# Performance work log

Hardware: AMD Instinct MI355X
Metric: run time of the kernel (lower is better)

Reference implementation:

```python
import jax, jax.numpy as jnp
import numpy as np

HEADS = 16
HEAD_DIM = 128


def rotate_half(x):
    x1, x2 = jnp.split(x, 2, axis=-1)
    return jnp.concatenate((-x2, x1), axis=-1)


def setup_inputs() -> dict:
    key = jax.random.key(0)
    ks = jax.random.split(key, 8)
    b, s, h = 2, 2048, 2048
    x = jax.random.normal(ks[0], (b, s, h), dtype=jnp.float32)
    attention_mask = jnp.zeros((1, 1, s, s), dtype=jnp.float32)
    alibi = jax.random.normal(ks[1], (1, HEADS, 1, s), dtype=jnp.float32)
    freqs = jax.random.normal(ks[2], (1, 1, s, HEAD_DIM), dtype=jnp.float32)
    scale = 1.0 / np.sqrt(h)
    Wq = jax.random.normal(ks[3], (h, h), dtype=jnp.float32) * scale
    Wk = jax.random.normal(ks[4], (h, h), dtype=jnp.float32) * scale
    Wv = jax.random.normal(ks[5], (h, h), dtype=jnp.float32) * scale
    Wo = jax.random.normal(ks[6], (h, h), dtype=jnp.float32) * scale
    return {"x": x, "attention_mask": attention_mask, "alibi": alibi,
            "freqs": freqs, "Wq": Wq, "Wk": Wk, "Wv": Wv, "Wo": Wo}


def reference(x, attention_mask, alibi, freqs, Wq, Wk, Wv, Wo):
    b, s, hidden = x.shape
    # torch Linear: y = x @ W.T (weight shape [out, in])
    def proj(W):
        y = x @ W.T
        return y.reshape(b, s, HEADS, HEAD_DIM).transpose(0, 2, 1, 3)  # [b,H,s,d]
    q, k, v = proj(Wq), proj(Wk), proj(Wv)
    cos, sin = jnp.cos(freqs), jnp.sin(freqs)
    q = q * cos + rotate_half(q) * sin
    k = k * cos + rotate_half(k) * sin
    scores = jnp.einsum('bhqd,bhkd->bhqk', q, k) / np.sqrt(HEAD_DIM)
    scores = scores + attention_mask + alibi
    attn = jax.nn.softmax(scores, axis=-1)
    out = jnp.einsum('bhqk,bhkd->bhqd', attn, v)
    out = out.transpose(0, 2, 1, 3).reshape(b, s, hidden)
    return out @ Wo.T
```

## Files before the change

kernel.cpp:

```cpp
#include <hip/hip_runtime.h>
#include <math.h>

typedef __attribute__((ext_vector_type(8))) short short8;
typedef __attribute__((ext_vector_type(4))) float f32x4;
typedef __attribute__((ext_vector_type(4))) unsigned short us4;
typedef __attribute__((ext_vector_type(4))) float fl4;

#define B_ 2
#define S_ 2048
#define H_ 16
#define D_ 128
#define HID 2048

__device__ __forceinline__ unsigned short f2bf(float f){
  unsigned u = __builtin_bit_cast(unsigned, f);
  u += 0x7fffu + ((u >> 16) & 1u);
  return (unsigned short)(u >> 16);
}
__device__ __forceinline__ float bf2f(unsigned short u){
  unsigned x = ((unsigned)u) << 16;
  return __builtin_bit_cast(float, x);
}
__device__ __forceinline__ int cvtpk(float lo, float hi){
  int r; asm("v_cvt_pk_bf16_f32 %0, %1, %2" : "=v"(r) : "v"(lo), "v"(hi)); return r;
}

__device__ __forceinline__ void g2lds16(const unsigned short* g, unsigned short* l){
  __builtin_amdgcn_global_load_lds(
      (const __attribute__((address_space(1))) unsigned int*)g,
      (__attribute__((address_space(3))) unsigned int*)l, 16, 0, 0);
}

__global__ void cvt_k(const float* __restrict__ src, unsigned short* __restrict__ dst){
  int i = (blockIdx.x * 256 + threadIdx.x) * 4;
  fl4 v = *(const fl4*)(src + i);
  us4 o;
  #pragma unroll
  for (int t = 0; t < 4; t++) o[t] = f2bf(v[t]);
  *(us4*)(dst + i) = o;
}

__global__ void tab_k(const float* __restrict__ freqs, float* __restrict__ ctab,
                      float* __restrict__ stab){
  int i = blockIdx.x * 256 + threadIdx.x;
  float f = freqs[i];
  ctab[i] = cosf(f);
  stab[i] = sinf(f);
}

template<int EPI>
__global__ __launch_bounds__(256) void gemm_k(
    const unsigned short* __restrict__ A,
    const unsigned short* __restrict__ B0,
    const unsigned short* __restrict__ B1,
    unsigned short* __restrict__ O0,
    unsigned short* __restrict__ O1,
    float* __restrict__ Of)
{
  __shared__ __align__(16) unsigned short As[2][128 * 32];
  __shared__ __align__(16) unsigned short Bs[2][128 * 32];
  const int tid = threadIdx.x;
  const int l = tid & 63, lg = l >> 4, lr = l & 15;
  const int w = tid >> 6, wm = w & 1, wn = w >> 1;
  const int m0 = blockIdx.x * 128, n0 = blockIdx.y * 128;
  const unsigned short* Bm = (EPI == 1 && blockIdx.z == 1) ? B1 : B0;

  f32x4 acc[4][4];
  #pragma unroll
  for (int i = 0; i < 4; i++)
    #pragma unroll
    for (int j = 0; j < 4; j++)
      acc[i][j] = f32x4{0.f, 0.f, 0.f, 0.f};

  const unsigned short* gA = A  + (size_t)(m0 + (tid >> 2)) * HID + (tid & 3) * 8;
  const unsigned short* gB = Bm + (size_t)(n0 + (tid >> 2)) * HID + (tid & 3) * 8;

  #define GSTAGE(buf, kt) do {                                   \
    g2lds16(gA + (kt),            As[buf] + tid * 8);            \
    g2lds16(gA + 64 * HID + (kt), As[buf] + 2048 + tid * 8);     \
    g2lds16(gB + (kt),            Bs[buf] + tid * 8);            \
    g2lds16(gB + 64 * HID + (kt), Bs[buf] + 2048 + tid * 8);     \
  } while (0)

  GSTAGE(0, 0);
  __syncthreads();
  int cur = 0;
  for (int t = 0; t < 64; t++){
    if (t < 63) GSTAGE(cur ^ 1, (t + 1) * 32);
    short8 aF[4], bF[4];
    #pragma unroll
    for (int mi = 0; mi < 4; mi++)
      aF[mi] = *(const short8*)(As[cur] + (wm * 64 + mi * 16 + lr) * 32 + lg * 8);
    #pragma unroll
    for (int ni = 0; ni < 4; ni++)
      bF[ni] = *(const short8*)(Bs[cur] + (wn * 64 + ni * 16 + lr) * 32 + lg * 8);
    #pragma unroll
    for (int mi = 0; mi < 4; mi++)
      #pragma unroll
      for (int ni = 0; ni < 4; ni++)
        acc[mi][ni] = __builtin_amdgcn_mfma_f32_16x16x32_bf16(aF[mi], bF[ni], acc[mi][ni], 0, 0, 0);
    __syncthreads();
    cur ^= 1;
  }
  #undef GSTAGE

  if (EPI == 1){
    unsigned short* O = blockIdx.z ? O1 : O0;
    #pragma unroll
    for (int mi = 0; mi < 4; mi++)
      #pragma unroll
      for (int r = 0; r < 4; r++){
        int i = m0 + wm * 64 + mi * 16 + lg * 4 + r;
        int b = i >> 11, s = i & 2047;
        #pragma unroll
        for (int ni = 0; ni < 4; ni++){
          int j = n0 + wn * 64 + ni * 16 + lr;
          int h = j >> 7, d = j & 127;
          O[((size_t)(b * H_ + h) * S_ + s) * D_ + d] = f2bf(acc[mi][ni][r]);
        }
      }
  } else if (EPI == 2){
    #pragma unroll
    for (int mi = 0; mi < 4; mi++)
      #pragma unroll
      for (int r = 0; r < 4; r++){
        int gi = m0 + wm * 64 + mi * 16 + lg * 4 + r;
        int h = gi >> 7, d = gi & 127;
        #pragma unroll
        for (int ni = 0; ni < 4; ni++){
          int gj = n0 + wn * 64 + ni * 16 + lr;
          int b = gj >> 11, s = gj & 2047;
          O0[((size_t)(b * H_ + h) * D_ + d) * S_ + s] = f2bf(acc[mi][ni][r]);
        }
      }
  } else {
    #pragma unroll
    for (int mi = 0; mi < 4; mi++)
      #pragma unroll
      for (int r = 0; r < 4; r++){
        int i = m0 + wm * 64 + mi * 16 + lg * 4 + r;
        #pragma unroll
        for (int ni = 0; ni < 4; ni++){
          int j = n0 + wn * 64 + ni * 16 + lr;
          Of[(size_t)i * HID + j] = acc[mi][ni][r];
        }
      }
  }
}

__global__ void rope_k(unsigned short* __restrict__ Q, unsigned short* __restrict__ K,
                       const float* __restrict__ ctab, const float* __restrict__ stab){
  int idx = blockIdx.x * 256 + threadIdx.x;
  unsigned short* P = (idx >= (1 << 20)) ? K : Q;
  int e  = idx & ((1 << 20) - 1);
  int g  = e & 15;
  int s  = (e >> 4) & 2047;
  int bh = e >> 15;
  int d0 = g * 4;
  size_t base = ((size_t)bh * S_ + s) * D_;
  us4 qa = *(us4*)(P + base + d0);
  us4 qb = *(us4*)(P + base + d0 + 64);
  fl4 ca = *(const fl4*)(ctab + s * D_ + d0);
  fl4 sa = *(const fl4*)(stab + s * D_ + d0);
  fl4 cb = *(const fl4*)(ctab + s * D_ + d0 + 64);
  fl4 sb = *(const fl4*)(stab + s * D_ + d0 + 64);
  us4 oa, ob;
  #pragma unroll
  for (int t = 0; t < 4; t++){
    float xa = bf2f(qa[t]), xb = bf2f(qb[t]);
    oa[t] = f2bf(xa * ca[t] - xb * sa[t]);
    ob[t] = f2bf(xb * cb[t] + xa * sb[t]);
  }
  *(us4*)(P + base + d0)      = oa;
  *(us4*)(P + base + d0 + 64) = ob;
}

__global__ __launch_bounds__(256) void attn_k(
    const unsigned short* __restrict__ Q,
    const unsigned short* __restrict__ Kg,
    const unsigned short* __restrict__ Vt,
    const float* __restrict__ mask,
    const float* __restrict__ alibi,
    unsigned short* __restrict__ Ctx)
{
  __shared__ __align__(16) unsigned short Kl[2][64 * 128];
  __shared__ __align__(16) unsigned short Vl[2][128 * 64];
  const int tid = threadIdx.x;
  const int l = tid & 63, lg = l >> 4, lr = l & 15;
  const int w = tid >> 6;
  const int bh = blockIdx.y, b = bh >> 4, h = bh & 15;
  const int q0 = blockIdx.x * 64 + w * 16;
  const size_t hb = (size_t)bh * S_ * D_;
  const float* mrow = mask + (size_t)(q0 + lr) * S_;
  const float* al = alibi + h * S_;
  const int sidx = (l & 48) + ((l & 48) >> 2);
  const float SCL2E = 0.08838834764831845f * 1.4426950408889634f;
  const float L2E = 1.4426950408889634f;

  const int kswz = (((tid & 15) ^ ((tid >> 4) & 7)) * 8);
  const unsigned short* gK = Kg + hb + (size_t)(tid >> 4) * D_ + kswz;
  const int vswz = (((tid & 7) ^ ((tid >> 3) & 7)) * 8);
  const unsigned short* gV = Vt + hb + (size_t)(tid >> 3) * S_ + vswz;

  #define ASTAGE(buf, kv)  do {                                            \
    g2lds16(gK + (size_t)((kv))      * D_, Kl[buf] + tid * 8);             \
    g2lds16(gK + (size_t)((kv) + 16) * D_, Kl[buf] + 2048 + tid * 8);      \
    g2lds16(gK + (size_t)((kv) + 32) * D_, Kl[buf] + 4096 + tid * 8);      \
    g2lds16(gK + (size_t)((kv) + 48) * D_, Kl[buf] + 6144 + tid * 8);      \
    g2lds16(gV + (kv),                     Vl[buf] + tid * 8);             \
    g2lds16(gV + 32 * S_ + (kv),           Vl[buf] + 2048 + tid * 8);      \
    g2lds16(gV + 64 * S_ + (kv),           Vl[buf] + 4096 + tid * 8);      \
    g2lds16(gV + 96 * S_ + (kv),           Vl[buf] + 6144 + tid * 8);      \
  } while (0)

  int koff[4];
  #pragma unroll
  for (int c = 0; c < 4; c++) koff[c] = ((c * 4 + lg) ^ (lr & 7)) * 8;
  const int vo0 = (lg ^ (lr & 7)) * 8, vo1 = ((4 + lg) ^ (lr & 7)) * 8;

  short8 qf[4];
  #pragma unroll
  for (int c = 0; c < 4; c++)
    qf[c] = *(const short8*)(Q + hb + (size_t)(q0 + lr) * D_ + c * 32 + lg * 8);

  f32x4 acc[8];
  #pragma unroll
  for (int c = 0; c < 8; c++) acc[c] = f32x4{0.f, 0.f, 0.f, 0.f};
  float mr = -1e30f, lsum = 0.f;

  ASTAGE(0, 0);
  __syncthreads();
  int cur = 0;

  for (int t = 0; t < 32; t++){
    const int kv0 = t * 64;
    if (t < 31) ASTAGE(cur ^ 1, kv0 + 64);

    fl4 mk[4], aa[4];
    #pragma unroll
    for (int g = 0; g < 4; g++){
      mk[g] = *(const fl4*)(mrow + kv0 + g * 16 + 4 * lg);
      aa[g] = *(const fl4*)(al  + kv0 + g * 16 + 4 * lg);
    }

    f32x4 sg[4];
    #pragma unroll
    for (int g = 0; g < 4; g++) sg[g] = f32x4{0.f, 0.f, 0.f, 0.f};
    #pragma unroll
    for (int g = 0; g < 4; g++){
      const int row = g * 16 + lr;
      #pragma unroll
      for (int c = 0; c < 4; c++){
        short8 kf = *(const short8*)(Kl[cur] + row * 128 + koff[c]);
        sg[g] = __builtin_amdgcn_mfma_f32_16x16x32_bf16(kf, qf[c], sg[g], 0, 0, 0);
      }
    }

    float x[4][4];
    #pragma unroll
    for (int g = 0; g < 4; g++)
      #pragma unroll
      for (int r = 0; r < 4; r++)
        x[g][r] = fmaf(sg[g][r], SCL2E, (mk[g][r] + aa[g][r]) * L2E);

    float mx = -1e30f;
    #pragma unroll
    for (int g = 0; g < 4; g++)
      #pragma unroll
      for (int r = 0; r < 4; r++) mx = fmaxf(mx, x[g][r]);

    float p[4][4], ps = 0.f;
    if (__all(mx <= mr + 8.f)){
      #pragma unroll
      for (int g = 0; g < 4; g++)
        #pragma unroll
        for (int r = 0; r < 4; r++){
          p[g][r] = exp2f(x[g][r] - mr);
          ps += p[g][r];
        }
      ps += __shfl_xor(ps, 16);
      ps += __shfl_xor(ps, 32);
      lsum += ps;
    } else {
      mx = fmaxf(mx, __shfl_xor(mx, 16));
      mx = fmaxf(mx, __shfl_xor(mx, 32));
      float mnew = fmaxf(mr, mx);
      float alpha = exp2f(mr - mnew);
      #pragma unroll
      for (int g = 0; g < 4; g++)
        #pragma unroll
        for (int r = 0; r < 4; r++){
          p[g][r] = exp2f(x[g][r] - mnew);
          ps += p[g][r];
        }
      ps += __shfl_xor(ps, 16);
      ps += __shfl_xor(ps, 32);
      lsum = lsum * alpha + ps;
      mr = mnew;
      float ar[4];
      #pragma unroll
      for (int r = 0; r < 4; r++) ar[r] = __shfl(alpha, sidx + r);
      #pragma unroll
      for (int c = 0; c < 8; c++)
        #pragma unroll
        for (int r = 0; r < 4; r++) acc[c][r] *= ar[r];
    }

    int pk0[4], pk1[4];
    #pragma unroll
    for (int r = 0; r < 4; r++){
      pk0[r] = cvtpk(p[0][r], p[1][r]);
      pk1[r] = cvtpk(p[2][r], p[3][r]);
    }

    const int srcb = lr + ((lg & 1) << 5);
    short8 af0, af1;
    #pragma unroll
    for (int j = 0; j < 8; j++){
      int w0 = __shfl(pk0[j & 3], srcb + ((j >> 2) << 4));
      int w1 = __shfl(pk1[j & 3], srcb + ((j >> 2) << 4));
      af0[j] = (short)((l & 32) ? ((unsigned)w0 >> 16) : ((unsigned)w0 & 0xffffu));
      af1[j] = (short)((l & 32) ? ((unsigned)w1 >> 16) : ((unsigned)w1 & 0xffffu));
    }

    #pragma unroll
    for (int c = 0; c < 8; c++){
      const int d0 = c * 16 + lr;
      short8 vf0 = *(const short8*)(Vl[cur] + d0 * 64 + vo0);
      short8 vf1 = *(const short8*)(Vl[cur] + d0 * 64 + vo1);
      acc[c] = __builtin_amdgcn_mfma_f32_16x16x32_bf16(af0, vf0, acc[c], 0, 0, 0);
      acc[c] = __builtin_amdgcn_mfma_f32_16x16x32_bf16(af1, vf1, acc[c], 0, 0, 0);
    }

    __syncthreads();
    cur ^= 1;
  }
  #undef ASTAGE

  float inv = 1.f / lsum;
  float ir[4];
  #pragma unroll
  for (int r = 0; r < 4; r++) ir[r] = __shfl(inv, sidx + r);
  #pragma unroll
  for (int r = 0; r < 4; r++){
    const int qg = q0 + 4 * lg + r;
    const size_t ob = ((size_t)(b * S_ + qg) * H_ + h) * D_;
    #pragma unroll
    for (int c = 0; c < 8; c++)
      Ctx[ob + c * 16 + lr] = f2bf(acc[c][r] * ir[r]);
  }
}

extern "C" void kernel_launch(void* const* d_in, const int* in_sizes, int n_in,
                              void* d_out, int out_size, void* d_ws, size_t ws_size,
                              hipStream_t stream){
  const float* x     = (const float*)d_in[0];
  const float* mask  = (const float*)d_in[1];
  const float* alibi = (const float*)d_in[2];
  const float* freqs = (const float*)d_in[3];
  const float* Wq    = (const float*)d_in[4];
  const float* Wk    = (const float*)d_in[5];
  const float* Wv    = (const float*)d_in[6];
  const float* Wo    = (const float*)d_in[7];
  float* out = (float*)d_out;

  unsigned short* ws  = (unsigned short*)d_ws;
  unsigned short* xb  = ws;
  unsigned short* wqb = ws + 8388608;
  unsigned short* wkb = ws + 12582912;
  unsigned short* wvb = ws + 16777216;
  unsigned short* wob = ws + 20971520;
  unsigned short* Qb  = ws + 25165824;
  unsigned short* Kb  = ws + 33554432;
  unsigned short* Vb  = ws + 41943040;
  unsigned short* ctx = xb;
  float* ctab = (float*)(ws + 50331648);
  float* stab = ctab + 262144;

  cvt_k<<<8192, 256, 0, stream>>>(x,  xb);
  cvt_k<<<4096, 256, 0, stream>>>(Wq, wqb);
  cvt_k<<<4096, 256, 0, stream>>>(Wk, wkb);
  cvt_k<<<4096, 256, 0, stream>>>(Wv, wvb);
  cvt_k<<<4096, 256, 0, stream>>>(Wo, wob);
  tab_k<<<1024, 256, 0, stream>>>(freqs, ctab, stab);

  gemm_k<1><<<dim3(32, 16, 2), 256, 0, stream>>>(xb, wqb, wkb, Qb, Kb, nullptr);
  gemm_k<2><<<dim3(16, 32, 1), 256, 0, stream>>>(wvb, xb, nullptr, Vb, nullptr, nullptr);
  rope_k<<<8192, 256, 0, stream>>>(Qb, Kb, ctab, stab);
  attn_k<<<dim3(32, 32), 256, 0, stream>>>(Qb, Kb, Vb, mask, alibi, ctx);
  gemm_k<0><<<dim3(32, 16, 1), 256, 0, stream>>>(ctx, wob, nullptr, nullptr, nullptr, out);
}
```

Before: 562.3 us.

## Remap block indices for XCD locality and widen attention blocks to 128 queries

GEMM and attention grids become 1D and are remapped so that consecutive blocks dispatched to the same XCD (stride 8) share row and column tiles or heads, which should improve L2 reuse. The attention kernel moves to 512 threads with 8 waves covering 128 query rows. K/V tiles are now shared by twice as many queries, and the staging loads drop from four to two per thread. The larger block uses more threads per CU and may lower occupancy.

```diff
diff --git a/kernel.cpp b/kernel.cpp
--- a/kernel.cpp
+++ b/kernel.cpp
@@ -62,8 +62,14 @@
   const int tid = threadIdx.x;
   const int l = tid & 63, lg = l >> 4, lr = l & 15;
   const int w = tid >> 6, wm = w & 1, wn = w >> 1;
-  const int m0 = blockIdx.x * 128, n0 = blockIdx.y * 128;
-  const unsigned short* Bm = (EPI == 1 && blockIdx.z == 1) ? B1 : B0;
+
+  const int f = blockIdx.x;
+  int bx, by, z = 0;
+  if (EPI == 1){ int g = (f & 7) * 128 + (f >> 3); bx = g >> 5; int r = g & 31; by = r & 15; z = r >> 4; }
+  else if (EPI == 2){ int g = (f & 7) * 64 + (f >> 3); bx = g >> 5; by = g & 31; }
+  else { int g = (f & 7) * 64 + (f >> 3); by = g >> 5; bx = g & 31; }
+  const int m0 = bx * 128, n0 = by * 128;
+  const unsigned short* Bm = (EPI == 1 && z == 1) ? B1 : B0;
 
   f32x4 acc[4][4];
   #pragma unroll
@@ -105,7 +111,7 @@
   #undef GSTAGE
 
   if (EPI == 1){
-    unsigned short* O = blockIdx.z ? O1 : O0;
+    unsigned short* O = z ? O1 : O0;
     #pragma unroll
     for (int mi = 0; mi < 4; mi++)
       #pragma unroll
@@ -175,7 +181,7 @@
   *(us4*)(P + base + d0 + 64) = ob;
 }
 
-__global__ __launch_bounds__(256) void attn_k(
+__global__ __launch_bounds__(512) void attn_k(
     const unsigned short* __restrict__ Q,
     const unsigned short* __restrict__ Kg,
     const unsigned short* __restrict__ Vt,
@@ -188,8 +194,11 @@
   const int tid = threadIdx.x;
   const int l = tid & 63, lg = l >> 4, lr = l & 15;
   const int w = tid >> 6;
-  const int bh = blockIdx.y, b = bh >> 4, h = bh & 15;
-  const int q0 = blockIdx.x * 64 + w * 16;
+  const int f = blockIdx.x;
+  const int g = (f & 7) * 64 + (f >> 3);
+  const int bh = g >> 4, qx = g & 15;
+  const int b = bh >> 4, h = bh & 15;
+  const int q0 = qx * 128 + w * 16;
   const size_t hb = (size_t)bh * S_ * D_;
   const float* mrow = mask + (size_t)(q0 + lr) * S_;
   const float* al = alibi + h * S_;
@@ -197,20 +206,16 @@
   const float SCL2E = 0.08838834764831845f * 1.4426950408889634f;
   const float L2E = 1.4426950408889634f;
 
-  const int kswz = (((tid & 15) ^ ((tid >> 4) & 7)) * 8);
-  const unsigned short* gK = Kg + hb + (size_t)(tid >> 4) * D_ + kswz;
-  const int vswz = (((tid & 7) ^ ((tid >> 3) & 7)) * 8);
-  const unsigned short* gV = Vt + hb + (size_t)(tid >> 3) * S_ + vswz;
+  const unsigned short* gK = Kg + hb + (size_t)(tid >> 4) * D_
+                             + (((tid & 15) ^ ((tid >> 4) & 7)) * 8);
+  const unsigned short* gV = Vt + hb + (size_t)(tid >> 3) * S_
+                             + (((tid & 7) ^ ((tid >> 3) & 7)) * 8);
 
   #define ASTAGE(buf, kv)  do {                                            \
-    g2lds16(gK + (size_t)((kv))      * D_, Kl[buf] + tid * 8);             \
-    g2lds16(gK + (size_t)((kv) + 16) * D_, Kl[buf] + 2048 + tid * 8);      \
+    g2lds16(gK + (size_t)(kv) * D_,        Kl[buf] + tid * 8);             \
     g2lds16(gK + (size_t)((kv) + 32) * D_, Kl[buf] + 4096 + tid * 8);      \
-    g2lds16(gK + (size_t)((kv) + 48) * D_, Kl[buf] + 6144 + tid * 8);      \
     g2lds16(gV + (kv),                     Vl[buf] + tid * 8);             \
-    g2lds16(gV + 32 * S_ + (kv),           Vl[buf] + 2048 + tid * 8);      \
     g2lds16(gV + 64 * S_ + (kv),           Vl[buf] + 4096 + tid * 8);      \
-    g2lds16(gV + 96 * S_ + (kv),           Vl[buf] + 6144 + tid * 8);      \
   } while (0)
 
   int koff[4];
@@ -238,45 +243,45 @@
 
     fl4 mk[4], aa[4];
     #pragma unroll
-    for (int g = 0; g < 4; g++){
-      mk[g] = *(const fl4*)(mrow + kv0 + g * 16 + 4 * lg);
-      aa[g] = *(const fl4*)(al  + kv0 + g * 16 + 4 * lg);
+    for (int g2 = 0; g2 < 4; g2++){
+      mk[g2] = *(const fl4*)(mrow + kv0 + g2 * 16 + 4 * lg);
+      aa[g2] = *(const fl4*)(al  + kv0 + g2 * 16 + 4 * lg);
     }
 
     f32x4 sg[4];
     #pragma unroll
-    for (int g = 0; g < 4; g++) sg[g] = f32x4{0.f, 0.f, 0.f, 0.f};
-    #pragma unroll
-    for (int g = 0; g < 4; g++){
-      const int row = g * 16 + lr;
+    for (int g2 = 0; g2 < 4; g2++) sg[g2] = f32x4{0.f, 0.f, 0.f, 0.f};
+    #pragma unroll
+    for (int g2 = 0; g2 < 4; g2++){
+      const int row = g2 * 16 + lr;
       #pragma unroll
       for (int c = 0; c < 4; c++){
         short8 kf = *(const short8*)(Kl[cur] + row * 128 + koff[c]);
-        sg[g] = __builtin_amdgcn_mfma_f32_16x16x32_bf16(kf, qf[c], sg[g], 0, 0, 0);
+        sg[g2] = __builtin_amdgcn_mfma_f32_16x16x32_bf16(kf, qf[c], sg[g2], 0, 0, 0);
       }
     }
 
     float x[4][4];
     #pragma unroll
-    for (int g = 0; g < 4; g++)
+    for (int g2 = 0; g2 < 4; g2++)
       #pragma unroll
       for (int r = 0; r < 4; r++)
-        x[g][r] = fmaf(sg[g][r], SCL2E, (mk[g][r] + aa[g][r]) * L2E);
+        x[g2][r] = fmaf(sg[g2][r], SCL2E, (mk[g2][r] + aa[g2][r]) * L2E);
 
     float mx = -1e30f;
     #pragma unroll
-    for (int g = 0; g < 4; g++)
-      #pragma unroll
-      for (int r = 0; r < 4; r++) mx = fmaxf(mx, x[g][r]);
+    for (int g2 = 0; g2 < 4; g2++)
+      #pragma unroll
+      for (int r = 0; r < 4; r++) mx = fmaxf(mx, x[g2][r]);
 
     float p[4][4], ps = 0.f;
     if (__all(mx <= mr + 8.f)){
       #pragma unroll
-      for (int g = 0; g < 4; g++)
+      for (int g2 = 0; g2 < 4; g2++)
         #pragma unroll
         for (int r = 0; r < 4; r++){
-          p[g][r] = exp2f(x[g][r] - mr);
-          ps += p[g][r];
+          p[g2][r] = exp2f(x[g2][r] - mr);
+          ps += p[g2][r];
         }
       ps += __shfl_xor(ps, 16);
       ps += __shfl_xor(ps, 32);
@@ -287,11 +292,11 @@
       float mnew = fmaxf(mr, mx);
       float alpha = exp2f(mr - mnew);
       #pragma unroll
-      for (int g = 0; g < 4; g++)
+      for (int g2 = 0; g2 < 4; g2++)
         #pragma unroll
         for (int r = 0; r < 4; r++){
-          p[g][r] = exp2f(x[g][r] - mnew);
-          ps += p[g][r];
+          p[g2][r] = exp2f(x[g2][r] - mnew);
+          ps += p[g2][r];
         }
       ps += __shfl_xor(ps, 16);
       ps += __shfl_xor(ps, 32);
@@ -384,9 +389,9 @@
   cvt_k<<<4096, 256, 0, stream>>>(Wo, wob);
   tab_k<<<1024, 256, 0, stream>>>(freqs, ctab, stab);
 
-  gemm_k<1><<<dim3(32, 16, 2), 256, 0, stream>>>(xb, wqb, wkb, Qb, Kb, nullptr);
-  gemm_k<2><<<dim3(16, 32, 1), 256, 0, stream>>>(wvb, xb, nullptr, Vb, nullptr, nullptr);
+  gemm_k<1><<<1024, 256, 0, stream>>>(xb, wqb, wkb, Qb, Kb, nullptr);
+  gemm_k<2><<<512, 256, 0, stream>>>(wvb, xb, nullptr, Vb, nullptr, nullptr);
   rope_k<<<8192, 256, 0, stream>>>(Qb, Kb, ctab, stab);
-  attn_k<<<dim3(32, 32), 256, 0, stream>>>(Qb, Kb, Vb, mask, alibi, ctx);
-  gemm_k<0><<<dim3(32, 16, 1), 256, 0, stream>>>(ctx, wob, nullptr, nullptr, nullptr, out);
-}
+  attn_k<<<512, 512, 0, stream>>>(Qb, Kb, Vb, mask, alibi, ctx);
+  gemm_k<0><<<512, 256, 0, stream>>>(ctx, wob, nullptr, nullptr, nullptr, out);
+}
```

Result: slower. 592.2 us (+5.3%).

## Replace GEMM with 256x256-tile 8-wave pipelined kernel and fuse QKV projections

Applied to the files above, without the earlier changes.

The 128x128 4-wave GEMM is replaced by a 256x256-tile, 512-thread kernel with a swizzled 128KB LDS double buffer. It interleaves global-to-LDS staging with quadrant-wise MFMA phases, using explicit waitcnt, barriers and setprio. Q, K and V projections now run as one launch over blockIdx.z, with V written transposed through vectorized stores, and the output projection uses the same kernel. The aim is more data reuse per tile and better overlap of memory with MFMA. The cost is larger register and LDS use and fragile hand-tuned synchronization.

```diff
diff --git a/kernel.cpp b/kernel.cpp
--- a/kernel.cpp
+++ b/kernel.cpp
@@ -48,104 +48,138 @@
   stab[i] = sinf(f);
 }
 
+#define PHEND_VM  do { asm volatile("s_waitcnt vmcnt(6)" ::: "memory"); \
+  __builtin_amdgcn_sched_barrier(0); __builtin_amdgcn_s_barrier(); } while(0)
+#define PHEND     do { \
+  __builtin_amdgcn_sched_barrier(0); __builtin_amdgcn_s_barrier(); } while(0)
+#define PREBAR    __builtin_amdgcn_s_barrier()
+
+#define RD_A(slotb, half) do { _Pragma("unroll") \
+  for (int i = 0; i < 4; i++){ _Pragma("unroll") \
+    for (int ks = 0; ks < 2; ks++) \
+      a[i][ks] = *(const short8*)(L + (slotb) + (half)*8192 + abase + i*2048 + kg[ks]); } } while(0)
+
+#define RD_B(slotb, half) do { _Pragma("unroll") \
+  for (int n = 0; n < 2; n++){ _Pragma("unroll") \
+    for (int ks = 0; ks < 2; ks++) \
+      b[(half)*2+n][ks] = *(const short8*)(L + (slotb) + 16384 + (half)*8192 + bbase + n*4096 + kg[ks]); } } while(0)
+
+#define MMQ(X, Y) do { __builtin_amdgcn_s_setprio(1); _Pragma("unroll") \
+  for (int i = 0; i < 4; i++){ _Pragma("unroll") \
+    for (int n = 0; n < 2; n++){ _Pragma("unroll") \
+      for (int ks = 0; ks < 2; ks++) \
+        acc[(X)*4+i][(Y)*2+n] = __builtin_amdgcn_mfma_f32_16x16x32_bf16( \
+            a[i][ks], b[(Y)*2+n][ks], acc[(X)*4+i][(Y)*2+n], 0, 0, 0); } } \
+  __builtin_amdgcn_s_setprio(0); } while(0)
+
 template<int EPI>
-__global__ __launch_bounds__(256) void gemm_k(
+__global__ __launch_bounds__(512, 2) void gemm8_k(
     const unsigned short* __restrict__ A,
-    const unsigned short* __restrict__ B0,
-    const unsigned short* __restrict__ B1,
+    const unsigned short* __restrict__ W0,
+    const unsigned short* __restrict__ W1,
+    const unsigned short* __restrict__ W2,
     unsigned short* __restrict__ O0,
     unsigned short* __restrict__ O1,
+    unsigned short* __restrict__ O2,
     float* __restrict__ Of)
 {
-  __shared__ __align__(16) unsigned short As[2][128 * 32];
-  __shared__ __align__(16) unsigned short Bs[2][128 * 32];
+  __shared__ __align__(16) unsigned short L[2 * 4 * 8192];
   const int tid = threadIdx.x;
   const int l = tid & 63, lg = l >> 4, lr = l & 15;
-  const int w = tid >> 6, wm = w & 1, wn = w >> 1;
-  const int m0 = blockIdx.x * 128, n0 = blockIdx.y * 128;
-  const unsigned short* Bm = (EPI == 1 && blockIdx.z == 1) ? B1 : B0;
-
-  f32x4 acc[4][4];
-  #pragma unroll
-  for (int i = 0; i < 4; i++)
+  const int w = tid >> 6, wm = w >> 2, wn = w & 3;
+  const int m0 = blockIdx.x * 256, n0 = blockIdx.y * 256;
+  const int z = (EPI == 1) ? blockIdx.z : 0;
+  const unsigned short* Bop = (EPI == 1) ? (z == 0 ? W0 : (z == 1 ? W1 : W2)) : W0;
+
+  f32x4 acc[8][4];
+  #pragma unroll
+  for (int i = 0; i < 8; i++)
     #pragma unroll
     for (int j = 0; j < 4; j++)
       acc[i][j] = f32x4{0.f, 0.f, 0.f, 0.f};
 
-  const unsigned short* gA = A  + (size_t)(m0 + (tid >> 2)) * HID + (tid & 3) * 8;
-  const unsigned short* gB = Bm + (size_t)(n0 + (tid >> 2)) * HID + (tid & 3) * 8;
-
-  #define GSTAGE(buf, kt) do {                                   \
-    g2lds16(gA + (kt),            As[buf] + tid * 8);            \
-    g2lds16(gA + 64 * HID + (kt), As[buf] + 2048 + tid * 8);     \
-    g2lds16(gB + (kt),            Bs[buf] + tid * 8);            \
-    g2lds16(gB + 64 * HID + (kt), Bs[buf] + 2048 + tid * 8);     \
-  } while (0)
-
-  GSTAGE(0, 0);
-  __syncthreads();
-  int cur = 0;
-  for (int t = 0; t < 64; t++){
-    if (t < 63) GSTAGE(cur ^ 1, (t + 1) * 32);
-    short8 aF[4], bF[4];
-    #pragma unroll
-    for (int mi = 0; mi < 4; mi++)
-      aF[mi] = *(const short8*)(As[cur] + (wm * 64 + mi * 16 + lr) * 32 + lg * 8);
-    #pragma unroll
-    for (int ni = 0; ni < 4; ni++)
-      bF[ni] = *(const short8*)(Bs[cur] + (wn * 64 + ni * 16 + lr) * 32 + lg * 8);
-    #pragma unroll
-    for (int mi = 0; mi < 4; mi++)
-      #pragma unroll
-      for (int ni = 0; ni < 4; ni++)
-        acc[mi][ni] = __builtin_amdgcn_mfma_f32_16x16x32_bf16(aF[mi], bF[ni], acc[mi][ni], 0, 0, 0);
-    __syncthreads();
-    cur ^= 1;
+  const int gsw = (((tid & 7) ^ ((tid >> 3) & 7)) * 8);
+  const unsigned short* gA = A   + (size_t)(m0 + (tid >> 3)) * HID + gsw;
+  const unsigned short* gB = Bop + (size_t)(n0 + (tid >> 3)) * HID + gsw;
+  const size_t HIN = (size_t)64  * HID;
+  const size_t HB  = (size_t)128 * HID;
+
+  const int abase = (wm * 16 + lr) * 64;
+  const int bbase = (wn * 16 + lr) * 64;
+  int kg[2];
+  kg[0] = ((lg)     ^ (lr & 7)) * 8;
+  kg[1] = ((4 + lg) ^ (lr & 7)) * 8;
+
+  #define STG(gsrc, tile, ldst) do { \
+    const unsigned short* _s = (gsrc) + (size_t)(tile) * 64; \
+    g2lds16(_s,       (ldst) + tid * 8); \
+    g2lds16(_s + HIN, (ldst) + 4096 + tid * 8); } while(0)
+
+  short8 a[4][2], b[4][2];
+
+  STG(gA, 0, L);
+  STG(gA + HB, 0, L + 8192);
+  STG(gB, 0, L + 16384);
+  STG(gB + HB, 0, L + 24576);
+  asm volatile("s_waitcnt vmcnt(0)" ::: "memory");
+  __builtin_amdgcn_sched_barrier(0);
+  __builtin_amdgcn_s_barrier();
+  STG(gA, 1, L + 32768);
+
+  for (int it = 0; it < 16; ++it){
+    const int t1 = 2 * it + 1, t2 = 2 * it + 2, t3 = 2 * it + 3;
+    RD_A(0, 0); RD_B(0, 0);
+    STG(gB, t1, L + 32768 + 16384);
+    PREBAR; MMQ(0, 0); PHEND_VM;
+    RD_B(0, 1);
+    STG(gB + HB, t1, L + 32768 + 24576);
+    PREBAR; MMQ(0, 1); PHEND_VM;
+    RD_A(0, 1);
+    STG(gA + HB, t1, L + 32768 + 8192);
+    PREBAR; MMQ(1, 0); PHEND;
+    STG(gA, t2, L);
+    PREBAR; MMQ(1, 1); PHEND_VM;
+    RD_A(32768, 0); RD_B(32768, 0);
+    STG(gB, t2, L + 16384);
+    PREBAR; MMQ(0, 0); PHEND_VM;
+    RD_B(32768, 1);
+    STG(gB + HB, t2, L + 24576);
+    PREBAR; MMQ(0, 1); PHEND_VM;
+    RD_A(32768, 1);
+    STG(gA + HB, t2, L + 8192);
+    PREBAR; MMQ(1, 0); PHEND;
+    STG(gA, t3, L + 32768);
+    PREBAR; MMQ(1, 1); PHEND_VM;
   }
-  #undef GSTAGE
-
-  if (EPI == 1){
-    unsigned short* O = blockIdx.z ? O1 : O0;
-    #pragma unroll
-    for (int mi = 0; mi < 4; mi++)
-      #pragma unroll
-      for (int r = 0; r < 4; r++){
-        int i = m0 + wm * 64 + mi * 16 + lg * 4 + r;
-        int b = i >> 11, s = i & 2047;
-        #pragma unroll
-        for (int ni = 0; ni < 4; ni++){
-          int j = n0 + wn * 64 + ni * 16 + lr;
-          int h = j >> 7, d = j & 127;
-          O[((size_t)(b * H_ + h) * S_ + s) * D_ + d] = f2bf(acc[mi][ni][r]);
+  #undef STG
+
+  #pragma unroll
+  for (int mf = 0; mf < 8; mf++)
+    #pragma unroll
+    for (int nf = 0; nf < 4; nf++){
+      const int j = n0 + nf * 64 + wn * 16 + lr;
+      const int i0 = m0 + mf * 32 + wm * 16 + lg * 4;
+      if (EPI == 0){
+        #pragma unroll
+        for (int r = 0; r < 4; r++)
+          Of[(size_t)(i0 + r) * HID + j] = acc[mf][nf][r];
+      } else if (z == 2){
+        const int b = i0 >> 11, s = i0 & 2047, h = j >> 7, d = j & 127;
+        us4 v;
+        #pragma unroll
+        for (int r = 0; r < 4; r++) v[r] = f2bf(acc[mf][nf][r]);
+        *(us4*)(O2 + ((size_t)(b * H_ + h) * D_ + d) * S_ + s) = v;
+      } else {
+        unsigned short* O = z ? O1 : O0;
+        const int h = j >> 7, d = j & 127;
+        #pragma unroll
+        for (int r = 0; r < 4; r++){
+          const int i = i0 + r;
+          const int b = i >> 11, s = i & 2047;
+          O[((size_t)(b * H_ + h) * S_ + s) * D_ + d] = f2bf(acc[mf][nf][r]);
         }
       }
-  } else if (EPI == 2){
-    #pragma unroll
-    for (int mi = 0; mi < 4; mi++)
-      #pragma unroll
-      for (int r = 0; r < 4; r++){
-        int gi = m0 + wm * 64 + mi * 16 + lg * 4 + r;
-        int h = gi >> 7, d = gi & 127;
-        #pragma unroll
-        for (int ni = 0; ni < 4; ni++){
-          int gj = n0 + wn * 64 + ni * 16 + lr;
-          int b = gj >> 11, s = gj & 2047;
-          O0[((size_t)(b * H_ + h) * D_ + d) * S_ + s] = f2bf(acc[mi][ni][r]);
-        }
-      }
-  } else {
-    #pragma unroll
-    for (int mi = 0; mi < 4; mi++)
-      #pragma unroll
-      for (int r = 0; r < 4; r++){
-        int i = m0 + wm * 64 + mi * 16 + lg * 4 + r;
-        #pragma unroll
-        for (int ni = 0; ni < 4; ni++){
-          int j = n0 + wn * 64 + ni * 16 + lr;
-          Of[(size_t)i * HID + j] = acc[mi][ni][r];
-        }
-      }
-  }
+    }
 }
 
 __global__ void rope_k(unsigned short* __restrict__ Q, unsigned short* __restrict__ K,
@@ -384,9 +418,10 @@
   cvt_k<<<4096, 256, 0, stream>>>(Wo, wob);
   tab_k<<<1024, 256, 0, stream>>>(freqs, ctab, stab);
 
-  gemm_k<1><<<dim3(32, 16, 2), 256, 0, stream>>>(xb, wqb, wkb, Qb, Kb, nullptr);
-  gemm_k<2><<<dim3(16, 32, 1), 256, 0, stream>>>(wvb, xb, nullptr, Vb, nullptr, nullptr);
+  gemm8_k<1><<<dim3(16, 8, 3), 512, 0, stream>>>(xb, wqb, wkb, wvb,
+                                                 Qb, Kb, Vb, nullptr);
   rope_k<<<8192, 256, 0, stream>>>(Qb, Kb, ctab, stab);
   attn_k<<<dim3(32, 32), 256, 0, stream>>>(Qb, Kb, Vb, mask, alibi, ctx);
-  gemm_k<0><<<dim3(32, 16, 1), 256, 0, stream>>>(ctx, wob, nullptr, nullptr, nullptr, out);
-}
+  gemm8_k<0><<<dim3(16, 8, 1), 512, 0, stream>>>(ctx, wob, nullptr, nullptr,
+                                                 nullptr, nullptr, nullptr, out);
+}
```

New measurement: 508.7 us. 1.11x faster.
